# Kernel optimization log

Hardware: AMD Instinct MI355X
Metric: run time of the kernel (lower is better)

Reference implementation:

```python
import jax, jax.numpy as jnp
import numpy as np

EMBED_DIM = 1024
NUM_HEADS = 16
HEAD_DIM = EMBED_DIM // NUM_HEADS
B, S = 4, 2048


def setup_inputs() -> dict:
    key = jax.random.key(0)
    ks = jax.random.split(key, 9)
    scale = 1.0 / np.sqrt(EMBED_DIM)
    inp = {
        "inputs": jax.random.normal(ks[0], (B, S, EMBED_DIM), dtype=jnp.float32),
        "rotation_params": jax.random.normal(ks[1], (B, S, EMBED_DIM), dtype=jnp.float32),
        "entangle_params": jax.random.normal(ks[2], (B, S, EMBED_DIM), dtype=jnp.float32),
        # Linear weights stored as (out, in) like torch; applied as x @ W.T
        "Wq": jax.random.normal(ks[3], (EMBED_DIM, EMBED_DIM), dtype=jnp.float32) * scale,
        "Wk": jax.random.normal(ks[4], (EMBED_DIM, EMBED_DIM), dtype=jnp.float32) * scale,
        "Wv": jax.random.normal(ks[5], (EMBED_DIM, EMBED_DIM), dtype=jnp.float32) * scale,
        "Wrot": jax.random.normal(ks[6], (EMBED_DIM, EMBED_DIM), dtype=jnp.float32) * scale,
        "Went": jax.random.normal(ks[7], (EMBED_DIM, EMBED_DIM), dtype=jnp.float32) * scale,
        "Wo": jax.random.normal(ks[8], (EMBED_DIM, EMBED_DIM), dtype=jnp.float32) * scale,
    }
    return inp


def _split_heads(x):
    b, s, e = x.shape
    return x.reshape(b, s, NUM_HEADS, HEAD_DIM).transpose(0, 2, 1, 3)  # (B,H,S,D)


def reference(inputs, rotation_params, entangle_params, Wq, Wk, Wv, Wrot, Went, Wo):
    Q = inputs @ Wq.T + rotation_params @ Wrot.T
    K = inputs @ Wk.T + entangle_params @ Went.T
    V = inputs @ Wv.T
    Qh, Kh, Vh = _split_heads(Q), _split_heads(K), _split_heads(V)
    scores = jnp.einsum("bhqd,bhkd->bhqk", Qh, Kh) / jnp.sqrt(jnp.float32(HEAD_DIM))
    attn = jax.nn.softmax(scores, axis=-1)  # dropout p=0 -> identity
    out = jnp.einsum("bhqk,bhkd->bhqd", attn, Vh)
    out = out.transpose(0, 2, 1, 3).reshape(inputs.shape[0], inputs.shape[1], EMBED_DIM)
    return out @ Wo.T
```

## Files before the change

### kernel.cpp

```cpp
#include <hip/hip_runtime.h>
#include <stdint.h>


typedef unsigned short u16;
typedef __bf16 bf16x8 __attribute__((ext_vector_type(8)));
typedef float f32x4 __attribute__((ext_vector_type(4)));
typedef float f32x16 __attribute__((ext_vector_type(16)));
typedef uint32_t u32x4 __attribute__((ext_vector_type(4)));

#define MFMA_BF16(a, b, c) __builtin_amdgcn_mfma_f32_16x16x32_bf16((a), (b), (c), 0, 0, 0)
#define MFMA32(a, b, c)    __builtin_amdgcn_mfma_f32_32x32x16_bf16((a), (b), (c), 0, 0, 0)
#define GAMMA 0.18033688011112042f
#define BHSTRIDE 131072
#define FENCE() __builtin_amdgcn_sched_barrier(0)

static __device__ __forceinline__ u16 f2bf(float f) {
    uint32_t u = __builtin_bit_cast(uint32_t, f);
    u = (u + 0x7FFFu + ((u >> 16) & 1u)) >> 16;
    return (u16)u;
}

static __device__ __forceinline__ uint32_t pk_rne2(float a, float b) {
    uint32_t ua = __builtin_bit_cast(uint32_t, a);
    uint32_t ub = __builtin_bit_cast(uint32_t, b);
    ua += 0x7FFFu + ((ua >> 16) & 1u);
    ub += 0x7FFFu + ((ub >> 16) & 1u);
    return __builtin_amdgcn_perm(ub, ua, 0x07060302);
}

static __device__ __forceinline__ void async_copy16(const void* g, void* l) {
    __builtin_amdgcn_global_load_lds((__attribute__((address_space(1))) void*)g,
                                     (__attribute__((address_space(3))) void*)l,
                                     16, 0, 0);
}

static __device__ __forceinline__ float aexp2(float x) {
    float r;
    asm("v_exp_f32 %0, %1" : "=v"(r) : "v"(x));
    return r;
}

static __device__ __forceinline__ uint32_t cvtpk(float a, float b) {
    uint32_t r;
    asm("v_cvt_pk_bf16_f32 %0, %1, %2" : "=v"(r) : "v"(a), "v"(b));
    return r;
}

static __device__ __forceinline__ void plswap(uint32_t& a, uint32_t& b) {
    asm("v_permlane32_swap_b32 %0, %1" : "+v"(a), "+v"(b));
}

static __device__ __forceinline__ bf16x8 mkfrag(uint32_t w0, uint32_t w1,
                                                uint32_t w2, uint32_t w3) {
    u32x4 u = {w0, w1, w2, w3};
    return __builtin_bit_cast(bf16x8, u);
}

struct CvtArgs { const float* s[9]; u16* d[9]; };

__global__ __launch_bounds__(256) void cvt_kernel(CvtArgs a) {
    if (blockIdx.z >= 3 && blockIdx.x >= 512) return;
    const float* s = a.s[blockIdx.z];
    u16* d = a.d[blockIdx.z];
    int i = (blockIdx.x * 256 + threadIdx.x) * 8;
    float4 f0 = *(const float4*)(s + i);
    float4 f1 = *(const float4*)(s + i + 4);
    uint4 w;
    w.x = pk_rne2(f0.x, f0.y); w.y = pk_rne2(f0.z, f0.w);
    w.z = pk_rne2(f1.x, f1.y); w.w = pk_rne2(f1.z, f1.w);
    *(uint4*)(d + i) = w;
}

__global__ __launch_bounds__(256, 3) void qkv_proj(
    const u16* __restrict__ Xb,
    const u16* __restrict__ Wqb, const u16* __restrict__ RVb,
    const u16* __restrict__ Wrotb, u16* __restrict__ Qhm,
    const u16* __restrict__ Wkb, const u16* __restrict__ EOb,
    const u16* __restrict__ Wentb, u16* __restrict__ Khm,
    const u16* __restrict__ Wvb, u16* __restrict__ Vt)
{
    __shared__ __align__(16) u16 lA[128 * 64];
    __shared__ __align__(16) u16 lB[128 * 64];

    const int tid  = threadIdx.x;
    const int lane = tid & 63;
    const int wave = tid >> 6;
    const int wm   = (wave >> 1) * 64;
    const int wn   = (wave & 1) * 64;
    const size_t m0 = (size_t)blockIdx.x * 128;

    const int sel = blockIdx.y >> 3;
    const size_t n0 = (size_t)(blockIdx.y & 7) * 128;
    const u16* W0 = sel == 0 ? Wqb : (sel == 1 ? Wkb : Wvb);
    const u16* A1 = sel == 1 ? EOb : RVb;
    const u16* W1 = sel == 1 ? Wentb : Wrotb;
    const float scale = sel == 0 ? GAMMA : 1.0f;
    const int npairs = sel == 2 ? 1 : 2;

    const int row8 = tid >> 3;
    const int cp   = tid & 7;
    const int fr   = lane & 15;
    const int g    = lane >> 4;

    f32x4 acc[4][4] = {};

    for (int p = 0; p < npairs; ++p) {
        const u16* A = p ? A1 : Xb;
        const u16* W = p ? W1 : W0;
        for (int k0 = 0; k0 < 1024; k0 += 64) {
            __syncthreads();
#pragma unroll
            for (int it = 0; it < 4; ++it) {
                int row = it * 32 + row8;
                int sc = cp ^ (((row >> 3) ^ row) & 7);
                async_copy16(A + ((m0 + row) * 1024 + k0 + sc * 8),
                             (char*)lA + it * 4096 + tid * 16);
                async_copy16(W + ((n0 + row) * 1024 + k0 + sc * 8),
                             (char*)lB + it * 4096 + tid * 16);
            }
            __syncthreads();

            bf16x8 af[4][2], bfm[4][2];
#pragma unroll
            for (int i = 0; i < 4; ++i) {
                int row = wm + i * 16 + fr;
                int sw = ((row >> 3) ^ row) & 7;
                af[i][0] = *(const bf16x8*)(lA + row * 64 + (g ^ sw) * 8);
                af[i][1] = *(const bf16x8*)(lA + row * 64 + ((4 + g) ^ sw) * 8);
            }
#pragma unroll
            for (int j = 0; j < 4; ++j) {
                int row = wn + j * 16 + fr;
                int sw = ((row >> 3) ^ row) & 7;
                bfm[j][0] = *(const bf16x8*)(lB + row * 64 + (g ^ sw) * 8);
                bfm[j][1] = *(const bf16x8*)(lB + row * 64 + ((4 + g) ^ sw) * 8);
            }
#pragma unroll
            for (int i = 0; i < 4; ++i)
#pragma unroll
                for (int j = 0; j < 4; ++j) {
                    acc[i][j] = MFMA_BF16(af[i][0], bfm[j][0], acc[i][j]);
                    acc[i][j] = MFMA_BF16(af[i][1], bfm[j][1], acc[i][j]);
                }
        }
    }

    if (sel == 2) {
#pragma unroll
        for (int i = 0; i < 4; ++i)
#pragma unroll
            for (int j = 0; j < 4; ++j) {
                size_t row0 = m0 + wm + i * 16 + g * 4;
                size_t col  = n0 + wn + j * 16 + fr;
                size_t addr = ((row0 >> 11) * 16 + (col >> 6)) * BHSTRIDE
                            + (size_t)(col & 63) * 2048 + (row0 & 2047);
                ushort4 pk;
                pk.x = f2bf(acc[i][j][0]);
                pk.y = f2bf(acc[i][j][1]);
                pk.z = f2bf(acc[i][j][2]);
                pk.w = f2bf(acc[i][j][3]);
                *(ushort4*)(Vt + addr) = pk;
            }
    } else {
        u16* C = sel == 0 ? Qhm : Khm;
#pragma unroll
        for (int i = 0; i < 4; ++i)
#pragma unroll
            for (int j = 0; j < 4; ++j)
#pragma unroll
                for (int rg = 0; rg < 4; ++rg) {
                    size_t row = m0 + wm + i * 16 + g * 4 + rg;
                    size_t col = n0 + wn + j * 16 + fr;
                    size_t addr = ((row >> 11) * 16 + (col >> 6)) * BHSTRIDE
                                + (row & 2047) * 64 + (col & 63);
                    C[addr] = f2bf(acc[i][j][rg] * scale);
                }
    }
}

__global__ __launch_bounds__(256, 3) void qk_proj(
    const u16* __restrict__ Xb,
    const u16* __restrict__ Wqb, const u16* __restrict__ RVb,
    const u16* __restrict__ Wrotb, u16* __restrict__ Qhm,
    const u16* __restrict__ Wkb, const u16* __restrict__ EOb,
    const u16* __restrict__ Wentb, u16* __restrict__ Khm)
{
    __shared__ __align__(16) u16 lA[128 * 64];
    __shared__ __align__(16) u16 lB[128 * 64];

    const int tid  = threadIdx.x;
    const int lane = tid & 63;
    const int wave = tid >> 6;
    const int wm   = (wave >> 1) * 64;
    const int wn   = (wave & 1) * 64;
    const size_t m0 = (size_t)blockIdx.x * 128;

    const bool isK = blockIdx.y >= 8;
    const size_t n0 = (size_t)(blockIdx.y & 7) * 128;
    const u16* W0 = isK ? Wkb  : Wqb;
    const u16* A1 = isK ? EOb  : RVb;
    const u16* W1 = isK ? Wentb : Wrotb;
    u16*       C  = isK ? Khm  : Qhm;
    const float scale = isK ? 1.0f : GAMMA;

    const int row8 = tid >> 3;
    const int cp   = tid & 7;
    const int fr   = lane & 15;
    const int g    = lane >> 4;

    f32x4 acc[4][4] = {};

    for (int p = 0; p < 2; ++p) {
        const u16* A = p ? A1 : Xb;
        const u16* W = p ? W1 : W0;
        for (int k0 = 0; k0 < 1024; k0 += 64) {
            __syncthreads();
#pragma unroll
            for (int it = 0; it < 4; ++it) {
                int row = it * 32 + row8;
                int sc = cp ^ (((row >> 3) ^ row) & 7);
                async_copy16(A + ((m0 + row) * 1024 + k0 + sc * 8),
                             (char*)lA + it * 4096 + tid * 16);
                async_copy16(W + ((n0 + row) * 1024 + k0 + sc * 8),
                             (char*)lB + it * 4096 + tid * 16);
            }
            __syncthreads();

            bf16x8 af[4][2], bfm[4][2];
#pragma unroll
            for (int i = 0; i < 4; ++i) {
                int row = wm + i * 16 + fr;
                int sw = ((row >> 3) ^ row) & 7;
                af[i][0] = *(const bf16x8*)(lA + row * 64 + (g ^ sw) * 8);
                af[i][1] = *(const bf16x8*)(lA + row * 64 + ((4 + g) ^ sw) * 8);
            }
#pragma unroll
            for (int j = 0; j < 4; ++j) {
                int row = wn + j * 16 + fr;
                int sw = ((row >> 3) ^ row) & 7;
                bfm[j][0] = *(const bf16x8*)(lB + row * 64 + (g ^ sw) * 8);
                bfm[j][1] = *(const bf16x8*)(lB + row * 64 + ((4 + g) ^ sw) * 8);
            }
#pragma unroll
            for (int i = 0; i < 4; ++i)
#pragma unroll
                for (int j = 0; j < 4; ++j) {
                    acc[i][j] = MFMA_BF16(af[i][0], bfm[j][0], acc[i][j]);
                    acc[i][j] = MFMA_BF16(af[i][1], bfm[j][1], acc[i][j]);
                }
        }
    }

#pragma unroll
    for (int i = 0; i < 4; ++i)
#pragma unroll
        for (int j = 0; j < 4; ++j)
#pragma unroll
            for (int rg = 0; rg < 4; ++rg) {
                size_t row = m0 + wm + i * 16 + g * 4 + rg;
                size_t col = n0 + wn + j * 16 + fr;
                size_t addr = ((row >> 11) * 16 + (col >> 6)) * BHSTRIDE
                            + (row & 2047) * 64 + (col & 63);
                C[addr] = f2bf(acc[i][j][rg] * scale);
            }
}

template <int AMODE, int CMODE>
__global__ __launch_bounds__(256, 2) void gemm_bt(
    const u16* __restrict__ A0, const u16* __restrict__ W0,
    const u16* __restrict__ A1, const u16* __restrict__ W1,
    void* __restrict__ Cv, int K, int npairs, float scale)
{
    __shared__ __align__(16) u16 lA[128 * 64];
    __shared__ __align__(16) u16 lB[128 * 64];

    const int tid  = threadIdx.x;
    const int lane = tid & 63;
    const int wave = tid >> 6;
    const int wm   = (wave >> 1) * 64;
    const int wn   = (wave & 1) * 64;
    const size_t m0 = (size_t)blockIdx.x * 128;
    const size_t n0 = (size_t)blockIdx.y * 128;

    const int row8 = tid >> 3;
    const int cp   = tid & 7;
    const int fr   = lane & 15;
    const int g    = lane >> 4;

    const size_t bb = (m0 >> 11) * 16;
    const size_t s0 = m0 & 2047;

    f32x4 acc[4][4] = {};

    for (int p = 0; p < npairs; ++p) {
        const u16* A = p ? A1 : A0;
        const u16* W = p ? W1 : W0;
        for (int k0 = 0; k0 < K; k0 += 64) {
            __syncthreads();
#pragma unroll
            for (int it = 0; it < 4; ++it) {
                int row = it * 32 + row8;
                int sc = cp ^ (((row >> 3) ^ row) & 7);
                if (AMODE == 0) {
                    async_copy16(A + ((m0 + row) * (size_t)K + k0 + sc * 8),
                                 (char*)lA + it * 4096 + tid * 16);
                } else {
                    size_t base = (bb + (size_t)(k0 >> 6)) * BHSTRIDE;
                    async_copy16(A + base + (s0 + row) * 64 + sc * 8,
                                 (char*)lA + it * 4096 + tid * 16);
                }
                async_copy16(W + ((n0 + row) * (size_t)K + k0 + sc * 8),
                             (char*)lB + it * 4096 + tid * 16);
            }
            __syncthreads();

            bf16x8 af[4][2], bfm[4][2];
#pragma unroll
            for (int i = 0; i < 4; ++i) {
                int row = wm + i * 16 + fr;
                int sw = ((row >> 3) ^ row) & 7;
                af[i][0] = *(const bf16x8*)(lA + row * 64 + (g ^ sw) * 8);
                af[i][1] = *(const bf16x8*)(lA + row * 64 + ((4 + g) ^ sw) * 8);
            }
#pragma unroll
            for (int j = 0; j < 4; ++j) {
                int row = wn + j * 16 + fr;
                int sw = ((row >> 3) ^ row) & 7;
                bfm[j][0] = *(const bf16x8*)(lB + row * 64 + (g ^ sw) * 8);
                bfm[j][1] = *(const bf16x8*)(lB + row * 64 + ((4 + g) ^ sw) * 8);
            }
#pragma unroll
            for (int i = 0; i < 4; ++i)
#pragma unroll
                for (int j = 0; j < 4; ++j) {
                    acc[i][j] = MFMA_BF16(af[i][0], bfm[j][0], acc[i][j]);
                    acc[i][j] = MFMA_BF16(af[i][1], bfm[j][1], acc[i][j]);
                }
        }
    }

#pragma unroll
    for (int i = 0; i < 4; ++i)
#pragma unroll
        for (int j = 0; j < 4; ++j) {
            if (CMODE == 2) {
                size_t row0 = m0 + wm + i * 16 + g * 4;
                size_t col  = n0 + wn + j * 16 + fr;
                size_t addr = ((row0 >> 11) * 16 + (col >> 6)) * BHSTRIDE
                            + (size_t)(col & 63) * 2048 + (row0 & 2047);
                ushort4 pk;
                pk.x = f2bf(acc[i][j][0] * scale);
                pk.y = f2bf(acc[i][j][1] * scale);
                pk.z = f2bf(acc[i][j][2] * scale);
                pk.w = f2bf(acc[i][j][3] * scale);
                *(ushort4*)((u16*)Cv + addr) = pk;
            } else {
#pragma unroll
                for (int rg = 0; rg < 4; ++rg) {
                    size_t row = m0 + wm + i * 16 + g * 4 + rg;
                    size_t col = n0 + wn + j * 16 + fr;
                    float v = acc[i][j][rg] * scale;
                    if (CMODE == 0) {
                        ((float*)Cv)[row * 1024 + col] = v;
                    } else {
                        size_t addr = ((row >> 11) * 16 + (col >> 6)) * BHSTRIDE
                                    + (row & 2047) * 64 + (col & 63);
                        ((u16*)Cv)[addr] = f2bf(v);
                    }
                }
            }
        }
}

__global__ __launch_bounds__(256, 2) void flash_kernel(
    const u16* __restrict__ Qhm, const u16* __restrict__ Khm,
    const u16* __restrict__ Vt, u16* __restrict__ Ohm)
{
    __shared__ __align__(16) u16 sK[2][128 * 64];
    __shared__ __align__(16) u16 sVt[2][64 * 128];

    const int tid  = threadIdx.x;
    const int lane = tid & 63;
    const int wave = tid >> 6;
    const int l31  = lane & 31;
    const int hg   = lane >> 5;

    const int lin  = blockIdx.x;
    const int slot = lin >> 3;
    const int bh   = (lin & 7) + 8 * (slot >> 3);
    const int q0   = (slot & 7) * 256;

    const u16* Qh = Qhm + (size_t)bh * BHSTRIDE;
    const u16* Kh = Khm + (size_t)bh * BHSTRIDE;
    const u16* Vh = Vt  + (size_t)bh * BHSTRIDE;
    u16*       Oh = Ohm + (size_t)bh * BHSTRIDE;

    bf16x8 qbf[2][4];
#pragma unroll
    for (int qt = 0; qt < 2; ++qt)
#pragma unroll
        for (int dc = 0; dc < 4; ++dc)
            qbf[qt][dc] = *(const bf16x8*)(Qh +
                (size_t)(q0 + wave * 64 + qt * 32 + l31) * 64 + dc * 16 + hg * 8);

    f32x16 oaccA[2] = {};
    f32x16 oaccB[2] = {};
    float lsA[2] = {}, lsB[2] = {};

    const int krow8 = tid >> 3, kcp = tid & 7;
    const int vd16  = tid >> 4, vcp = tid & 15;

    auto stage = [&](int buf, int kt) {
#pragma unroll
        for (int it = 0; it < 4; ++it) {
            int row = it * 32 + krow8;
            int sc = kcp ^ (((row >> 3) ^ row) & 7);
            async_copy16(Kh + (size_t)(kt * 128 + row) * 64 + sc * 8,
                         (char*)(&sK[buf][0]) + it * 4096 + tid * 16);
        }
#pragma unroll
        for (int it = 0; it < 4; ++it) {
            int d = it * 16 + vd16;
            int sc = vcp ^ (d & 15);
            async_copy16(Vh + (size_t)d * 2048 + kt * 128 + sc * 8,
                         (char*)(&sVt[buf][0]) + it * 4096 + tid * 16);
        }
    };

    auto qk2 = [&](const u16* sKc, int kc, f32x16& sa0, f32x16& sa1) {
        sa0 = (f32x16){};
        sa1 = (f32x16){};
        const int krow = kc * 32 + l31;
        const int ksw = ((krow >> 3) ^ krow) & 7;
#pragma unroll
        for (int dc = 0; dc < 4; ++dc) {
            bf16x8 ka = *(const bf16x8*)(sKc + krow * 64 + ((dc * 2 + hg) ^ ksw) * 8);
            sa0 = MFMA32(ka, qbf[0][dc], sa0);
            sa1 = MFMA32(ka, qbf[1][dc], sa1);
        }
    };

    auto sm = [&](const f32x16& sa, bf16x8& o0, bf16x8& o1, float* ls) {
        float p[16];
#pragma unroll
        for (int r = 0; r < 16; ++r) p[r] = aexp2(sa[r]);
#pragma unroll
        for (int r = 0; r < 16; ++r) ls[r & 1] += p[r];
        uint32_t w0 = cvtpk(p[0],  p[1]),  w1 = cvtpk(p[2],  p[3]);
        uint32_t w2 = cvtpk(p[4],  p[5]),  w3 = cvtpk(p[6],  p[7]);
        uint32_t w4 = cvtpk(p[8],  p[9]),  w5 = cvtpk(p[10], p[11]);
        uint32_t w6 = cvtpk(p[12], p[13]), w7 = cvtpk(p[14], p[15]);
        plswap(w0, w2); plswap(w1, w3);
        plswap(w4, w6); plswap(w5, w7);
        o0 = mkfrag(w0, w1, w2, w3);
        o1 = mkfrag(w4, w5, w6, w7);
    };

    auto pv2 = [&](const u16* sVc, int kc, bf16x8 a0, bf16x8 a1,
                   bf16x8 b0, bf16x8 b1) {
        bf16x8 vb[2][2];
#pragma unroll
        for (int sub = 0; sub < 2; ++sub)
#pragma unroll
            for (int dt = 0; dt < 2; ++dt) {
                int dr = dt * 32 + l31;
                vb[sub][dt] = *(const bf16x8*)(sVc + dr * 128 +
                    ((kc * 4 + sub * 2 + hg) ^ (dr & 15)) * 8);
            }
        oaccA[0] = MFMA32(a0, vb[0][0], oaccA[0]);
        oaccA[1] = MFMA32(a0, vb[0][1], oaccA[1]);
        oaccB[0] = MFMA32(b0, vb[0][0], oaccB[0]);
        oaccB[1] = MFMA32(b0, vb[0][1], oaccB[1]);
        oaccA[0] = MFMA32(a1, vb[1][0], oaccA[0]);
        oaccA[1] = MFMA32(a1, vb[1][1], oaccA[1]);
        oaccB[0] = MFMA32(b1, vb[1][0], oaccB[0]);
        oaccB[1] = MFMA32(b1, vb[1][1], oaccB[1]);
    };

    stage(0, 0);
    __syncthreads();

    int cur = 0;
    for (int kt = 0; kt < 16; ++kt) {
        const u16* sKc = &sK[cur][0];
        const u16* sVc = &sVt[cur][0];

        f32x16 sA, sB, nA, nB;
        qk2(sKc, 0, sA, sB);
        if (kt < 15) stage(cur ^ 1, kt + 1);
        FENCE();

        bf16x8 a0, a1, b0, b1;
        sm(sA, a0, a1, lsA);   FENCE();
        qk2(sKc, 1, nA, nB);   FENCE();
        sm(sB, b0, b1, lsB);   FENCE();
        pv2(sVc, 0, a0, a1, b0, b1); FENCE();
        sm(nA, a0, a1, lsA);   FENCE();
        qk2(sKc, 2, sA, sB);   FENCE();
        sm(nB, b0, b1, lsB);   FENCE();
        pv2(sVc, 1, a0, a1, b0, b1); FENCE();
        sm(sA, a0, a1, lsA);   FENCE();
        qk2(sKc, 3, nA, nB);   FENCE();
        sm(sB, b0, b1, lsB);   FENCE();
        pv2(sVc, 2, a0, a1, b0, b1); FENCE();
        sm(nA, a0, a1, lsA);   FENCE();
        sm(nB, b0, b1, lsB);   FENCE();
        pv2(sVc, 3, a0, a1, b0, b1);

        __syncthreads();
        cur ^= 1;
    }

#pragma unroll
    for (int qt = 0; qt < 2; ++qt) {
        float l = qt ? (lsB[0] + lsB[1]) : (lsA[0] + lsA[1]);
        l += __shfl_xor(l, 32);
        float inv = 1.0f / l;
        const f32x16* oa = qt ? oaccB : oaccA;
#pragma unroll
        for (int r = 0; r < 16; ++r) {
            int row = (r & 3) + 4 * hg + 8 * (r >> 2);
            float invr = __shfl(inv, row);
            size_t grow = (size_t)q0 + wave * 64 + qt * 32 + row;
            Oh[grow * 64 + l31]      = f2bf(oa[0][r] * invr);
            Oh[grow * 64 + 32 + l31] = f2bf(oa[1][r] * invr);
        }
    }
}

extern "C" void kernel_launch(void* const* d_in, const int* in_sizes, int n_in,
                              void* d_out, int out_size, void* d_ws, size_t ws_size,
                              hipStream_t stream)
{
    const float* X    = (const float*)d_in[0];
    const float* R    = (const float*)d_in[1];
    const float* E    = (const float*)d_in[2];
    const float* Wq   = (const float*)d_in[3];
    const float* Wk   = (const float*)d_in[4];
    const float* Wv   = (const float*)d_in[5];
    const float* Wrot = (const float*)d_in[6];
    const float* Went = (const float*)d_in[7];
    const float* Wo   = (const float*)d_in[8];

    const size_t NT = 8192 * 1024;
    const size_t NW = 1024 * 1024;

    u16* Qhm = (u16*)d_out;
    u16* Khm = Qhm + NT;
    u16* Xb  = (u16*)d_ws;
    u16* RVb = Xb + NT;
    u16* EOb = RVb + NT;
    u16* Wqb = EOb + NT;
    u16* Wkb   = Wqb + NW;
    u16* Wvb   = Wkb + NW;
    u16* Wrotb = Wvb + NW;
    u16* Wentb = Wrotb + NW;
    u16* Wob   = Wentb + NW;
    u16* VtX   = Wob + NW;

    const bool bigws = ws_size >= (4 * NT + 6 * NW) * sizeof(u16);
    u16* Vt = bigws ? VtX : RVb;

    {
        CvtArgs a{};
        a.s[0] = X;  a.s[1] = R;  a.s[2] = E;
        a.s[3] = Wq; a.s[4] = Wk; a.s[5] = Wv;
        a.s[6] = Wrot; a.s[7] = Went; a.s[8] = Wo;
        a.d[0] = Xb;  a.d[1] = RVb;  a.d[2] = EOb;
        a.d[3] = Wqb; a.d[4] = Wkb;  a.d[5] = Wvb;
        a.d[6] = Wrotb; a.d[7] = Wentb; a.d[8] = Wob;
        cvt_kernel<<<dim3(4096, 1, 9), 256, 0, stream>>>(a);
    }

    if (bigws) {
        qkv_proj<<<dim3(64, 24), 256, 0, stream>>>(Xb, Wqb, RVb, Wrotb, Qhm,
                                                   Wkb, EOb, Wentb, Khm,
                                                   Wvb, VtX);
    } else {
        qk_proj<<<dim3(64, 16), 256, 0, stream>>>(Xb, Wqb, RVb, Wrotb, Qhm,
                                                  Wkb, EOb, Wentb, Khm);
        gemm_bt<0, 2><<<dim3(64, 8), 256, 0, stream>>>(Xb, Wvb, nullptr, nullptr,
                                                       RVb, 1024, 1, 1.0f);
    }
    flash_kernel<<<dim3(512), 256, 0, stream>>>(Qhm, Khm, Vt, EOb);
    gemm_bt<1, 0><<<dim3(64, 8), 256, 0, stream>>>(EOb, Wob, nullptr, nullptr,
                                                   d_out, 1024, 1, 1.0f);
}
```

Before: 336.8 us.

## Shrink output-projection tile, raise qkv occupancy, prioritize MFMA waves in attention

Splits the templated GEMM into a dedicated V-projection fallback and a new output-projection kernel. The new kernel uses 128x64 tiles, giving 1024 blocks instead of 512, with a smaller register footprint and a 4-block-per-CU launch bound. It also raises qkv_proj's occupancy hint from 3 to 4 and wraps the flash-attention MFMA sequences in s_setprio so matrix work is scheduled ahead of softmax work. The trade-offs are more re-reading of the O tile across the doubled N blocks and possible register spilling at the higher occupancy targets.

```diff
diff --git a/kernel.cpp b/kernel.cpp
--- a/kernel.cpp
+++ b/kernel.cpp
@@ -71,7 +71,7 @@
     *(uint4*)(d + i) = w;
 }
 
-__global__ __launch_bounds__(256, 3) void qkv_proj(
+__global__ __launch_bounds__(256, 4) void qkv_proj(
     const u16* __restrict__ Xb,
     const u16* __restrict__ Wqb, const u16* __restrict__ RVb,
     const u16* __restrict__ Wrotb, u16* __restrict__ Qhm,
@@ -265,11 +265,9 @@
             }
 }
 
-template <int AMODE, int CMODE>
-__global__ __launch_bounds__(256, 2) void gemm_bt(
+__global__ __launch_bounds__(256, 2) void v_proj_fb(
     const u16* __restrict__ A0, const u16* __restrict__ W0,
-    const u16* __restrict__ A1, const u16* __restrict__ W1,
-    void* __restrict__ Cv, int K, int npairs, float scale)
+    u16* __restrict__ Cv)
 {
     __shared__ __align__(16) u16 lA[128 * 64];
     __shared__ __align__(16) u16 lB[128 * 64];
@@ -287,89 +285,140 @@
     const int fr   = lane & 15;
     const int g    = lane >> 4;
 
+    f32x4 acc[4][4] = {};
+
+    for (int k0 = 0; k0 < 1024; k0 += 64) {
+        __syncthreads();
+#pragma unroll
+        for (int it = 0; it < 4; ++it) {
+            int row = it * 32 + row8;
+            int sc = cp ^ (((row >> 3) ^ row) & 7);
+            async_copy16(A0 + ((m0 + row) * 1024 + k0 + sc * 8),
+                         (char*)lA + it * 4096 + tid * 16);
+            async_copy16(W0 + ((n0 + row) * 1024 + k0 + sc * 8),
+                         (char*)lB + it * 4096 + tid * 16);
+        }
+        __syncthreads();
+
+        bf16x8 af[4][2], bfm[4][2];
+#pragma unroll
+        for (int i = 0; i < 4; ++i) {
+            int row = wm + i * 16 + fr;
+            int sw = ((row >> 3) ^ row) & 7;
+            af[i][0] = *(const bf16x8*)(lA + row * 64 + (g ^ sw) * 8);
+            af[i][1] = *(const bf16x8*)(lA + row * 64 + ((4 + g) ^ sw) * 8);
+        }
+#pragma unroll
+        for (int j = 0; j < 4; ++j) {
+            int row = wn + j * 16 + fr;
+            int sw = ((row >> 3) ^ row) & 7;
+            bfm[j][0] = *(const bf16x8*)(lB + row * 64 + (g ^ sw) * 8);
+            bfm[j][1] = *(const bf16x8*)(lB + row * 64 + ((4 + g) ^ sw) * 8);
+        }
+#pragma unroll
+        for (int i = 0; i < 4; ++i)
+#pragma unroll
+            for (int j = 0; j < 4; ++j) {
+                acc[i][j] = MFMA_BF16(af[i][0], bfm[j][0], acc[i][j]);
+                acc[i][j] = MFMA_BF16(af[i][1], bfm[j][1], acc[i][j]);
+            }
+    }
+
+#pragma unroll
+    for (int i = 0; i < 4; ++i)
+#pragma unroll
+        for (int j = 0; j < 4; ++j) {
+            size_t row0 = m0 + wm + i * 16 + g * 4;
+            size_t col  = n0 + wn + j * 16 + fr;
+            size_t addr = ((row0 >> 11) * 16 + (col >> 6)) * BHSTRIDE
+                        + (size_t)(col & 63) * 2048 + (row0 & 2047);
+            ushort4 pk;
+            pk.x = f2bf(acc[i][j][0]);
+            pk.y = f2bf(acc[i][j][1]);
+            pk.z = f2bf(acc[i][j][2]);
+            pk.w = f2bf(acc[i][j][3]);
+            *(ushort4*)(Cv + addr) = pk;
+        }
+}
+
+__global__ __launch_bounds__(256, 4) void o_proj(
+    const u16* __restrict__ Ohm, const u16* __restrict__ Wob,
+    float* __restrict__ Out)
+{
+    __shared__ __align__(16) u16 lA[128 * 64];
+    __shared__ __align__(16) u16 lB[64 * 64];
+
+    const int tid  = threadIdx.x;
+    const int lane = tid & 63;
+    const int wave = tid >> 6;
+    const int wm   = (wave >> 1) * 64;
+    const int wn   = (wave & 1) * 32;
+    const size_t m0 = (size_t)blockIdx.x * 128;
+    const size_t n0 = (size_t)blockIdx.y * 64;
+
+    const int row8 = tid >> 3;
+    const int cp   = tid & 7;
+    const int fr   = lane & 15;
+    const int g    = lane >> 4;
+
     const size_t bb = (m0 >> 11) * 16;
     const size_t s0 = m0 & 2047;
 
-    f32x4 acc[4][4] = {};
-
-    for (int p = 0; p < npairs; ++p) {
-        const u16* A = p ? A1 : A0;
-        const u16* W = p ? W1 : W0;
-        for (int k0 = 0; k0 < K; k0 += 64) {
-            __syncthreads();
-#pragma unroll
-            for (int it = 0; it < 4; ++it) {
-                int row = it * 32 + row8;
-                int sc = cp ^ (((row >> 3) ^ row) & 7);
-                if (AMODE == 0) {
-                    async_copy16(A + ((m0 + row) * (size_t)K + k0 + sc * 8),
-                                 (char*)lA + it * 4096 + tid * 16);
-                } else {
-                    size_t base = (bb + (size_t)(k0 >> 6)) * BHSTRIDE;
-                    async_copy16(A + base + (s0 + row) * 64 + sc * 8,
-                                 (char*)lA + it * 4096 + tid * 16);
-                }
-                async_copy16(W + ((n0 + row) * (size_t)K + k0 + sc * 8),
-                             (char*)lB + it * 4096 + tid * 16);
-            }
-            __syncthreads();
-
-            bf16x8 af[4][2], bfm[4][2];
-#pragma unroll
-            for (int i = 0; i < 4; ++i) {
-                int row = wm + i * 16 + fr;
-                int sw = ((row >> 3) ^ row) & 7;
-                af[i][0] = *(const bf16x8*)(lA + row * 64 + (g ^ sw) * 8);
-                af[i][1] = *(const bf16x8*)(lA + row * 64 + ((4 + g) ^ sw) * 8);
-            }
-#pragma unroll
-            for (int j = 0; j < 4; ++j) {
-                int row = wn + j * 16 + fr;
-                int sw = ((row >> 3) ^ row) & 7;
-                bfm[j][0] = *(const bf16x8*)(lB + row * 64 + (g ^ sw) * 8);
-                bfm[j][1] = *(const bf16x8*)(lB + row * 64 + ((4 + g) ^ sw) * 8);
-            }
-#pragma unroll
-            for (int i = 0; i < 4; ++i)
-#pragma unroll
-                for (int j = 0; j < 4; ++j) {
-                    acc[i][j] = MFMA_BF16(af[i][0], bfm[j][0], acc[i][j]);
-                    acc[i][j] = MFMA_BF16(af[i][1], bfm[j][1], acc[i][j]);
-                }
-        }
+    f32x4 acc[4][2] = {};
+
+    for (int k0 = 0; k0 < 1024; k0 += 64) {
+        __syncthreads();
+        size_t base = (bb + (size_t)(k0 >> 6)) * BHSTRIDE;
+#pragma unroll
+        for (int it = 0; it < 4; ++it) {
+            int row = it * 32 + row8;
+            int sc = cp ^ (((row >> 3) ^ row) & 7);
+            async_copy16(Ohm + base + (s0 + row) * 64 + sc * 8,
+                         (char*)lA + it * 4096 + tid * 16);
+        }
+#pragma unroll
+        for (int it = 0; it < 2; ++it) {
+            int row = it * 32 + row8;
+            int sc = cp ^ (((row >> 3) ^ row) & 7);
+            async_copy16(Wob + ((n0 + row) * 1024 + k0 + sc * 8),
+                         (char*)lB + it * 4096 + tid * 16);
+        }
+        __syncthreads();
+
+        bf16x8 af[4][2], bfm[2][2];
+#pragma unroll
+        for (int i = 0; i < 4; ++i) {
+            int row = wm + i * 16 + fr;
+            int sw = ((row >> 3) ^ row) & 7;
+            af[i][0] = *(const bf16x8*)(lA + row * 64 + (g ^ sw) * 8);
+            af[i][1] = *(const bf16x8*)(lA + row * 64 + ((4 + g) ^ sw) * 8);
+        }
+#pragma unroll
+        for (int j = 0; j < 2; ++j) {
+            int row = wn + j * 16 + fr;
+            int sw = ((row >> 3) ^ row) & 7;
+            bfm[j][0] = *(const bf16x8*)(lB + row * 64 + (g ^ sw) * 8);
+            bfm[j][1] = *(const bf16x8*)(lB + row * 64 + ((4 + g) ^ sw) * 8);
+        }
+#pragma unroll
+        for (int i = 0; i < 4; ++i)
+#pragma unroll
+            for (int j = 0; j < 2; ++j) {
+                acc[i][j] = MFMA_BF16(af[i][0], bfm[j][0], acc[i][j]);
+                acc[i][j] = MFMA_BF16(af[i][1], bfm[j][1], acc[i][j]);
+            }
     }
 
 #pragma unroll
     for (int i = 0; i < 4; ++i)
 #pragma unroll
-        for (int j = 0; j < 4; ++j) {
-            if (CMODE == 2) {
-                size_t row0 = m0 + wm + i * 16 + g * 4;
-                size_t col  = n0 + wn + j * 16 + fr;
-                size_t addr = ((row0 >> 11) * 16 + (col >> 6)) * BHSTRIDE
-                            + (size_t)(col & 63) * 2048 + (row0 & 2047);
-                ushort4 pk;
-                pk.x = f2bf(acc[i][j][0] * scale);
-                pk.y = f2bf(acc[i][j][1] * scale);
-                pk.z = f2bf(acc[i][j][2] * scale);
-                pk.w = f2bf(acc[i][j][3] * scale);
-                *(ushort4*)((u16*)Cv + addr) = pk;
-            } else {
-#pragma unroll
-                for (int rg = 0; rg < 4; ++rg) {
-                    size_t row = m0 + wm + i * 16 + g * 4 + rg;
-                    size_t col = n0 + wn + j * 16 + fr;
-                    float v = acc[i][j][rg] * scale;
-                    if (CMODE == 0) {
-                        ((float*)Cv)[row * 1024 + col] = v;
-                    } else {
-                        size_t addr = ((row >> 11) * 16 + (col >> 6)) * BHSTRIDE
-                                    + (row & 2047) * 64 + (col & 63);
-                        ((u16*)Cv)[addr] = f2bf(v);
-                    }
-                }
-            }
-        }
+        for (int j = 0; j < 2; ++j)
+#pragma unroll
+            for (int rg = 0; rg < 4; ++rg) {
+                size_t row = m0 + wm + i * 16 + g * 4 + rg;
+                size_t col = n0 + wn + j * 16 + fr;
+                Out[row * 1024 + col] = acc[i][j][rg];
+            }
 }
 
 __global__ __launch_bounds__(256, 2) void flash_kernel(
@@ -432,12 +481,14 @@
         sa1 = (f32x16){};
         const int krow = kc * 32 + l31;
         const int ksw = ((krow >> 3) ^ krow) & 7;
+        __builtin_amdgcn_s_setprio(1);
 #pragma unroll
         for (int dc = 0; dc < 4; ++dc) {
             bf16x8 ka = *(const bf16x8*)(sKc + krow * 64 + ((dc * 2 + hg) ^ ksw) * 8);
             sa0 = MFMA32(ka, qbf[0][dc], sa0);
             sa1 = MFMA32(ka, qbf[1][dc], sa1);
         }
+        __builtin_amdgcn_s_setprio(0);
     };
 
     auto sm = [&](const f32x16& sa, bf16x8& o0, bf16x8& o1, float* ls) {
@@ -467,6 +518,7 @@
                 vb[sub][dt] = *(const bf16x8*)(sVc + dr * 128 +
                     ((kc * 4 + sub * 2 + hg) ^ (dr & 15)) * 8);
             }
+        __builtin_amdgcn_s_setprio(1);
         oaccA[0] = MFMA32(a0, vb[0][0], oaccA[0]);
         oaccA[1] = MFMA32(a0, vb[0][1], oaccA[1]);
         oaccB[0] = MFMA32(b0, vb[0][0], oaccB[0]);
@@ -475,6 +527,7 @@
         oaccA[1] = MFMA32(a1, vb[1][1], oaccA[1]);
         oaccB[0] = MFMA32(b1, vb[1][0], oaccB[0]);
         oaccB[1] = MFMA32(b1, vb[1][1], oaccB[1]);
+        __builtin_amdgcn_s_setprio(0);
     };
 
     stage(0, 0);
@@ -579,10 +632,8 @@
     } else {
         qk_proj<<<dim3(64, 16), 256, 0, stream>>>(Xb, Wqb, RVb, Wrotb, Qhm,
                                                   Wkb, EOb, Wentb, Khm);
-        gemm_bt<0, 2><<<dim3(64, 8), 256, 0, stream>>>(Xb, Wvb, nullptr, nullptr,
-                                                       RVb, 1024, 1, 1.0f);
+        v_proj_fb<<<dim3(64, 8), 256, 0, stream>>>(Xb, Wvb, RVb);
     }
     flash_kernel<<<dim3(512), 256, 0, stream>>>(Qhm, Khm, Vt, EOb);
-    gemm_bt<1, 0><<<dim3(64, 8), 256, 0, stream>>>(EOb, Wob, nullptr, nullptr,
-                                                   d_out, 1024, 1, 1.0f);
-}
+    o_proj<<<dim3(64, 16), 256, 0, stream>>>(EOb, Wob, (float*)d_out);
+}
```

After: 345.9 us. 1.03x slower.
